# Performance work log

Measured on AMD Instinct MI355X. Metric: run time of the kernel, lower is better.

## Reference

```python
import jax, jax.numpy as jnp
import numpy as np

B, T, E, H = 2, 2048, 1024, 16
D = E // H  # head dim = 64
ROPE_BASE = 10000.0


def setup_inputs() -> dict:
    key = jax.random.key(0)
    k0, k1, k2 = jax.random.split(key, 3)
    s = 0.02  # GPT-style init scale
    return {
        "x": jax.random.normal(k0, (B, T, E), jnp.float32),
        "w_qkv": jax.random.normal(k1, (E, 3 * E), jnp.float32) * s,
        "b_qkv": jnp.zeros((3 * E,), jnp.float32),
        "w_out": jax.random.normal(k2, (E, E), jnp.float32) * s,
        "b_out": jnp.zeros((E,), jnp.float32),
    }


def _rope_tables(t, d, dtype):
    # Llama rotary with scale=1 (YaRN degenerates to vanilla RoPE)
    inv_freq = 1.0 / (ROPE_BASE ** (jnp.arange(0, d, 2, dtype=jnp.float32) / d))
    freqs = jnp.arange(t, dtype=jnp.float32)[:, None] * inv_freq[None, :]  # [T, D/2]
    emb = jnp.concatenate([freqs, freqs], axis=-1)  # [T, D]
    return jnp.cos(emb).astype(dtype), jnp.sin(emb).astype(dtype)


def _rotate_half(x):
    return jnp.concatenate([-x[..., D // 2:], x[..., : D // 2]], axis=-1)


def reference(x, w_qkv, b_qkv, w_out, b_out):
    # 1) fused QKV projection
    qkv = x @ w_qkv + b_qkv                      # [B, T, 3E]
    q, k, v = jnp.split(qkv, 3, axis=-1)

    def heads(t):
        return t.reshape(B, T, H, D).transpose(0, 2, 1, 3)  # [B, H, T, D]

    q, k, v = heads(q), heads(k), heads(v)

    # 2) rotary position embedding on q, k
    cos, sin = _rope_tables(T, D, x.dtype)       # [T, D], broadcasts over B, H
    q = q * cos + _rotate_half(q) * sin
    k = k * cos + _rotate_half(k) * sin

    # 3) causal scaled dot-product attention
    scale = jnp.asarray(1.0 / np.sqrt(D), x.dtype)
    scores = jnp.einsum("bhqd,bhkd->bhqk", q, k) * scale
    causal = jnp.tril(jnp.ones((T, T), dtype=bool))
    scores = jnp.where(causal, scores, jnp.finfo(scores.dtype).min)
    attn = jax.nn.softmax(scores, axis=-1)
    out = jnp.einsum("bhqk,bhkd->bhqd", attn, v)  # [B, H, T, D]

    # 4) merge heads + output projection
    out = out.transpose(0, 2, 1, 3).reshape(B, T, E)
    return out @ w_out + b_out
```

## Files before the change

### kernel.cpp

```cpp
#include <hip/hip_runtime.h>
#include <hip/hip_bf16.h>
#include <stdint.h>

#define B_  2
#define T_  2048
#define E_  1024
#define H_  16
#define D_  64
#define BH_ 32

typedef unsigned short ushort_t;
typedef __attribute__((ext_vector_type(8))) short bfrag;
typedef __attribute__((ext_vector_type(4))) short s16x4;
typedef __attribute__((ext_vector_type(4))) float f32x4;

__device__ __forceinline__ ushort_t f2b(float f) {
    uint32_t u = __builtin_bit_cast(uint32_t, f);
    u += 0x7fffu + ((u >> 16) & 1u);
    return (ushort_t)(u >> 16);
}

#if defined(__has_builtin)
#if __has_builtin(__builtin_amdgcn_exp2f)
#define EXP2(x) __builtin_amdgcn_exp2f(x)
#endif
#endif
#ifndef EXP2
__device__ __forceinline__ float hexp2_(float x) {
    float r;
    asm volatile("v_exp_f32 %0, %1\n\ts_nop 1" : "=v"(r) : "v"(x));
    return r;
}
#define EXP2(x) hexp2_(x)
#endif

__device__ __forceinline__ uint32_t cvtpk_bf16(float lo, float hi) {
    uint32_t r;
    asm("v_cvt_pk_bf16_f32 %0, %1, %2" : "=v"(r) : "v"(lo), "v"(hi));
    return r;
}

typedef const __attribute__((address_space(1))) uint8_t* gas_t;
typedef __attribute__((address_space(3))) uint8_t* las_t;
__device__ __forceinline__ void gload_lds16(const void* g, void* l) {
    __builtin_amdgcn_global_load_lds((gas_t)g, (las_t)l, 16, 0, 0);
}
__device__ __forceinline__ void drain_vmem() {
    asm volatile("s_waitcnt vmcnt(0)" ::: "memory");
    __builtin_amdgcn_sched_barrier(0);
}

__global__ __launch_bounds__(256) void prep_kernel(const float* __restrict__ x, const float* __restrict__ w_qkv,
                                                   const float* __restrict__ w_out, ushort_t* __restrict__ xb,
                                                   ushort_t* __restrict__ wqkvT, ushort_t* __restrict__ woutT,
                                                   float2* __restrict__ cstab) {
    __shared__ float tile[32][36];
    int blk = blockIdx.x, tid = threadIdx.x;
    if (blk < 256) {
        int id = blk * 256 + tid;
        int j = id & 31, t = id >> 5;
        float ang = (float)t * expf(-(float)j * 0.2878231366242558f);
        float s, c;
        sincosf(ang, &s, &c);
        cstab[id] = make_float2(c, s);
    } else if (blk < 2304) {
        int i = ((blk - 256) * 256 + tid) * 8;
        float4 a = *(const float4*)(x + i);
        float4 b = *(const float4*)(x + i + 4);
        ushort_t r[8] = {f2b(a.x), f2b(a.y), f2b(a.z), f2b(a.w), f2b(b.x), f2b(b.y), f2b(b.z), f2b(b.w)};
        *(uint4*)(xb + i) = *(const uint4*)r;
    } else {
        const float* in;
        ushort_t* out;
        int R, C, bx, by;
        if (blk < 5376) { in = w_qkv; out = wqkvT; R = 1024; C = 3072; int t = blk - 2304; bx = t % 96; by = t / 96; }
        else            { in = w_out; out = woutT; R = 1024; C = 1024; int t = blk - 5376; bx = t % 32; by = t / 32; }
        int c0 = bx * 32, r0 = by * 32;
        int ty = tid >> 3, tx = tid & 7;
        float4 v = *(const float4*)&in[(size_t)(r0 + ty) * C + c0 + tx * 4];
        *(float4*)&tile[ty][tx * 4] = v;
        __syncthreads();
        int cc = tid & 31, rq = tid >> 5;
        float t0 = tile[rq * 4 + 0][cc], t1 = tile[rq * 4 + 1][cc];
        float t2 = tile[rq * 4 + 2][cc], t3 = tile[rq * 4 + 3][cc];
        uint2 w;
        w.x = cvtpk_bf16(t0, t1);
        w.y = cvtpk_bf16(t2, t3);
        *(uint2*)&out[(size_t)(c0 + cc) * R + r0 + rq * 4] = w;
    }
}

__global__ __launch_bounds__(256) void gemm_qkv_kernel(const ushort_t* __restrict__ A, const ushort_t* __restrict__ Bt,
                                                       const float* __restrict__ bias, const float2* __restrict__ cstab,
                                                       ushort_t* __restrict__ qw, ushort_t* __restrict__ kw,
                                                       ushort_t* __restrict__ vw) {
    const int K = 1024;
    __shared__ ushort_t As[128 * 64];
    __shared__ ushort_t Bs[128 * 64];
    int tid = threadIdx.x, lane = tid & 63, wid = tid >> 6;
    int lm = lane & 15, lg = lane >> 4;
    int bid = blockIdx.x;
    int xcd = bid & 7, idx = bid >> 3;
    int bm = xcd * 4 + idx / 24;
    int bn = idx % 24;
    int wm = wid >> 1, wn = wid & 1;

    int cbase = bn * 128 + wn * 64;
    bool qk = (cbase < 2048);

    f32x4 acc[4][4] = {};
    const ushort_t* ag = A + (size_t)bm * 128 * K;
    const ushort_t* bg = Bt + (size_t)bn * 128 * K;

    for (int kt = 0; kt < K / 64; ++kt) {
        __syncthreads();
#pragma unroll
        for (int c = 0; c < 4; ++c) {
            int G = c * 256 + tid;
            int rr = G >> 3;
            int gs = (G & 7) ^ (rr & 7);
            gload_lds16(ag + (size_t)rr * K + kt * 64 + gs * 8, As + (c * 256 + wid * 64) * 8);
            gload_lds16(bg + (size_t)rr * K + kt * 64 + gs * 8, Bs + (c * 256 + wid * 64) * 8);
        }
        __syncthreads();
        bfrag a[2][4], b[2][4];
#pragma unroll
        for (int kk = 0; kk < 2; ++kk) {
#pragma unroll
            for (int mi = 0; mi < 4; ++mi) {
                int row = wm * 64 + mi * 16 + lm;
                int slot = (kk * 4 + lg) ^ (lm & 7);
                a[kk][mi] = *(const bfrag*)&As[row * 64 + slot * 8];
            }
#pragma unroll
            for (int ni = 0; ni < 4; ++ni) {
                int row = wn * 64 + ni * 16 + lm;
                int slot = (kk * 4 + lg) ^ (lm & 7);
                b[kk][ni] = *(const bfrag*)&Bs[row * 64 + slot * 8];
            }
        }
        if (qk) {
#pragma unroll
            for (int kk = 0; kk < 2; ++kk)
#pragma unroll
                for (int mi = 0; mi < 4; ++mi)
#pragma unroll
                    for (int ni = 0; ni < 4; ++ni)
                        acc[mi][ni] = __builtin_amdgcn_mfma_f32_16x16x32_bf16(b[kk][ni], a[kk][mi], acc[mi][ni], 0, 0, 0);
        } else {
#pragma unroll
            for (int kk = 0; kk < 2; ++kk)
#pragma unroll
                for (int mi = 0; mi < 4; ++mi)
#pragma unroll
                    for (int ni = 0; ni < 4; ++ni)
                        acc[mi][ni] = __builtin_amdgcn_mfma_f32_16x16x32_bf16(a[kk][mi], b[kk][ni], acc[mi][ni], 0, 0, 0);
        }
    }

    int sel = cbase >> 10;
    int h = (cbase & 1023) >> 6;
    if (qk) {
        ushort_t* dst = sel ? kw : qw;
        float scale = sel ? 1.0f : 0.18033688011112042f;
        float4 bias4[4];
#pragma unroll
        for (int ni = 0; ni < 4; ++ni)
            bias4[ni] = *(const float4*)&bias[cbase + ni * 16 + lg * 4];
#pragma unroll
        for (int mi = 0; mi < 4; ++mi) {
            int r = bm * 128 + wm * 64 + mi * 16 + lm;
            int bb = r >> 11, t = r & (T_ - 1);
            size_t rowbase = ((size_t)(bb * H_ + h) * T_ + t) * D_;
#pragma unroll
            for (int nip = 0; nip < 2; ++nip) {
                const float4* cs2 = (const float4*)(cstab + t * 32 + nip * 16 + lg * 4);
                float4 ca = cs2[0], cb = cs2[1];
                float xl[4], xh[4];
#pragma unroll
                for (int i = 0; i < 4; ++i) {
                    xl[i] = acc[mi][nip][i]     + ((const float*)&bias4[nip])[i];
                    xh[i] = acc[mi][nip + 2][i] + ((const float*)&bias4[nip + 2])[i];
                }
                float rl0 = (xl[0] * ca.x - xh[0] * ca.y) * scale;
                float rl1 = (xl[1] * ca.z - xh[1] * ca.w) * scale;
                float rl2 = (xl[2] * cb.x - xh[2] * cb.y) * scale;
                float rl3 = (xl[3] * cb.z - xh[3] * cb.w) * scale;
                float rh0 = (xh[0] * ca.x + xl[0] * ca.y) * scale;
                float rh1 = (xh[1] * ca.z + xl[1] * ca.w) * scale;
                float rh2 = (xh[2] * cb.x + xl[2] * cb.y) * scale;
                float rh3 = (xh[3] * cb.z + xl[3] * cb.w) * scale;
                uint2 wlo, whi;
                wlo.x = cvtpk_bf16(rl0, rl1); wlo.y = cvtpk_bf16(rl2, rl3);
                whi.x = cvtpk_bf16(rh0, rh1); whi.y = cvtpk_bf16(rh2, rh3);
                *(uint2*)&dst[rowbase + nip * 16 + lg * 4]      = wlo;
                *(uint2*)&dst[rowbase + 32 + nip * 16 + lg * 4] = whi;
            }
        }
    } else {
        float bb4[4];
#pragma unroll
        for (int ni = 0; ni < 4; ++ni) bb4[ni] = bias[cbase + ni * 16 + lm];
#pragma unroll
        for (int ni = 0; ni < 4; ++ni) {
            int d = ni * 16 + lm;
#pragma unroll
            for (int mi = 0; mi < 4; ++mi) {
                int r = bm * 128 + wm * 64 + mi * 16 + lg * 4;
                int bb = r >> 11, tq = r & (T_ - 1);
                uint2 w;
                w.x = cvtpk_bf16(acc[mi][ni][0] + bb4[ni], acc[mi][ni][1] + bb4[ni]);
                w.y = cvtpk_bf16(acc[mi][ni][2] + bb4[ni], acc[mi][ni][3] + bb4[ni]);
                *(uint2*)&vw[((size_t)(bb * H_ + h) * D_ + d) * T_ + tq] = w;
            }
        }
    }
}

__global__ __launch_bounds__(256, 2) void flash_kernel(const ushort_t* __restrict__ q, const ushort_t* __restrict__ k,
                                                       const ushort_t* __restrict__ vt, ushort_t* __restrict__ o) {
    __shared__ ushort_t smemK[128 * 64];
    __shared__ ushort_t smemV[64 * 128];
    int tid = threadIdx.x, lane = tid & 63, wid = tid >> 6;
    int lm = lane & 15, lg = lane >> 4;
    int x = blockIdx.x & 7, r = blockIdx.x >> 3;
    int half = r >> 5, idx = r & 31;
    int bh = x * 4 + (idx & 3);
    int jq = idx >> 2;
    int j = half ? jq : 15 - jq;
    int q0w = j * 128 + wid * 32;
    int b = bh >> 4, h = bh & 15;
    int nt = j + 1;

    const ushort_t* qb = q + (size_t)bh * T_ * D_;
    const ushort_t* kb = k + (size_t)bh * T_ * D_;
    const ushort_t* vb = vt + (size_t)bh * D_ * T_;

    bfrag aq[2][2];
#pragma unroll
    for (int s = 0; s < 2; ++s)
#pragma unroll
        for (int hh = 0; hh < 2; ++hh)
            aq[s][hh] = *(const bfrag*)(qb + (size_t)(q0w + s * 16 + lm) * D_ + hh * 32 + lg * 8);

    f32x4 acc[2][4] = {};
    float lsum[2] = {0.f, 0.f};

    for (int t = 0; t < nt; ++t) {
        int k0 = t * 128;
        __syncthreads();
#pragma unroll
        for (int c = 0; c < 4; ++c) {
            int G = c * 256 + tid;
            int rrk = G >> 3, gk = (G & 7) ^ (rrk & 7);
            gload_lds16(kb + (size_t)(k0 + rrk) * D_ + gk * 8, smemK + (c * 256 + wid * 64) * 8);
            int rrv = G >> 4, gv = (G & 15) ^ (rrv & 7);
            gload_lds16(vb + (size_t)rrv * T_ + k0 + gv * 8, smemV + (c * 256 + wid * 64) * 8);
        }
        drain_vmem();
        __syncthreads();

        for (int h1 = 0; h1 < 2; ++h1) {
            int hk0 = k0 + h1 * 64;
            if (hk0 > q0w + 31) continue;
            bfrag ka[4][2];
#pragma unroll
            for (int sb = 0; sb < 4; ++sb)
#pragma unroll
                for (int hh = 0; hh < 2; ++hh) {
                    int krr = h1 * 64 + sb * 16 + lm;
                    int gr = (hh * 4 + lg) ^ (krr & 7);
                    ka[sb][hh] = *(const bfrag*)&smemK[krr * 64 + gr * 8];
                }
            s16x4 vq[4][4];
#pragma unroll
            for (int qq = 0; qq < 4; ++qq)
#pragma unroll
                for (int db = 0; db < 4; ++db) {
                    int rr = db * 16 + lm;
                    int g = h1 * 8 + qq * 2 + (lg >> 1);
                    int p = g ^ (rr & 7);
                    vq[qq][db] = *(const s16x4*)&smemV[rr * 128 + p * 8 + (lg & 1) * 4];
                }
            f32x4 st[2][4];
#pragma unroll
            for (int s = 0; s < 2; ++s)
#pragma unroll
                for (int sb = 0; sb < 4; ++sb) {
                    f32x4 z = {};
                    z = __builtin_amdgcn_mfma_f32_16x16x32_bf16(ka[sb][0], aq[s][0], z, 0, 0, 0);
                    st[s][sb] = __builtin_amdgcn_mfma_f32_16x16x32_bf16(ka[sb][1], aq[s][1], z, 0, 0, 0);
                }
            if (hk0 + 63 > q0w) {
#pragma unroll
                for (int s = 0; s < 2; ++s)
#pragma unroll
                    for (int sb = 0; sb < 4; ++sb)
#pragma unroll
                        for (int i = 0; i < 4; ++i)
                            if (hk0 + sb * 16 + lg * 4 + i > q0w + s * 16 + lm) st[s][sb][i] = -1e30f;
            }
#pragma unroll
            for (int s = 0; s < 2; ++s) {
                float pv[4][4];
#pragma unroll
                for (int sb = 0; sb < 4; ++sb)
#pragma unroll
                    for (int i = 0; i < 4; ++i)
                        pv[sb][i] = EXP2(st[s][sb][i]);
                lsum[s] += ((pv[0][0] + pv[0][1]) + (pv[0][2] + pv[0][3])) +
                           ((pv[1][0] + pv[1][1]) + (pv[1][2] + pv[1][3])) +
                           ((pv[2][0] + pv[2][1]) + (pv[2][2] + pv[2][3])) +
                           ((pv[3][0] + pv[3][1]) + (pv[3][2] + pv[3][3]));
                uint4 u0, u1;
                u0.x = cvtpk_bf16(pv[0][0], pv[0][1]);
                u0.y = cvtpk_bf16(pv[0][2], pv[0][3]);
                u0.z = cvtpk_bf16(pv[1][0], pv[1][1]);
                u0.w = cvtpk_bf16(pv[1][2], pv[1][3]);
                u1.x = cvtpk_bf16(pv[2][0], pv[2][1]);
                u1.y = cvtpk_bf16(pv[2][2], pv[2][3]);
                u1.z = cvtpk_bf16(pv[3][0], pv[3][1]);
                u1.w = cvtpk_bf16(pv[3][2], pv[3][3]);
                bfrag pf0 = __builtin_bit_cast(bfrag, u0);
                bfrag pf1 = __builtin_bit_cast(bfrag, u1);
#pragma unroll
                for (int db = 0; db < 4; ++db) {
                    bfrag va01 = __builtin_shufflevector(vq[0][db], vq[1][db], 0, 1, 2, 3, 4, 5, 6, 7);
                    bfrag va23 = __builtin_shufflevector(vq[2][db], vq[3][db], 0, 1, 2, 3, 4, 5, 6, 7);
                    acc[s][db] = __builtin_amdgcn_mfma_f32_16x16x32_bf16(va01, pf0, acc[s][db], 0, 0, 0);
                    acc[s][db] = __builtin_amdgcn_mfma_f32_16x16x32_bf16(va23, pf1, acc[s][db], 0, 0, 0);
                }
            }
        }
    }

#pragma unroll
    for (int s = 0; s < 2; ++s) {
        float lM = lsum[s];
        lM += __shfl_xor(lM, 16);
        lM += __shfl_xor(lM, 32);
        float inv = 1.0f / lM;
        int tq = q0w + s * 16 + lm;
        size_t ro = ((size_t)b * T_ + tq) * E_ + h * D_;
#pragma unroll
        for (int db = 0; db < 4; ++db) {
            uint2 w;
            w.x = cvtpk_bf16(acc[s][db][0] * inv, acc[s][db][1] * inv);
            w.y = cvtpk_bf16(acc[s][db][2] * inv, acc[s][db][3] * inv);
            *(uint2*)(o + ro + db * 16 + lg * 4) = w;
        }
    }
}

__global__ __launch_bounds__(256) void gemm_out_kernel(const ushort_t* __restrict__ A, const ushort_t* __restrict__ Bt,
                                                       const float* __restrict__ bias, float* __restrict__ out) {
    const int K = 1024;
    __shared__ ushort_t As[2][128 * 64];
    __shared__ ushort_t Bs[2][64 * 64];
    int tid = threadIdx.x, lane = tid & 63, wid = tid >> 6;
    int lm = lane & 15, lg = lane >> 4;
    int bid = blockIdx.x;
    int xcd = bid & 7, idx = bid >> 3;
    int bm = xcd * 4 + idx / 16;
    int bn = idx % 16;

    f32x4 acc[2][4] = {};
    const ushort_t* ag = A + (size_t)bm * 128 * K;
    const ushort_t* bg = Bt + (size_t)bn * 64 * K;

#define OUT_STAGE(kt_, buf_)                                                              \
    _Pragma("unroll")                                                                     \
    for (int c = 0; c < 4; ++c) {                                                         \
        int G = c * 256 + tid;                                                            \
        int rr = G >> 3;                                                                  \
        int gs = (G & 7) ^ (rr & 7);                                                      \
        gload_lds16(ag + (size_t)rr * K + (kt_) * 64 + gs * 8, &As[buf_][(c * 256 + wid * 64) * 8]); \
    }                                                                                     \
    _Pragma("unroll")                                                                     \
    for (int c = 0; c < 2; ++c) {                                                         \
        int G = c * 256 + tid;                                                            \
        int rr = G >> 3;                                                                  \
        int gs = (G & 7) ^ (rr & 7);                                                      \
        gload_lds16(bg + (size_t)rr * K + (kt_) * 64 + gs * 8, &Bs[buf_][(c * 256 + wid * 64) * 8]); \
    }

    int cur = 0;
    OUT_STAGE(0, 0);
    drain_vmem();
    __syncthreads();

    for (int kt = 0; kt < K / 64; ++kt) {
        if (kt + 1 < K / 64) { OUT_STAGE(kt + 1, cur ^ 1); }
        bfrag a[2][2], b[2][4];
#pragma unroll
        for (int kk = 0; kk < 2; ++kk) {
#pragma unroll
            for (int mi = 0; mi < 2; ++mi) {
                int row = wid * 32 + mi * 16 + lm;
                int slot = (kk * 4 + lg) ^ (lm & 7);
                a[kk][mi] = *(const bfrag*)&As[cur][row * 64 + slot * 8];
            }
#pragma unroll
            for (int ni = 0; ni < 4; ++ni) {
                int row = ni * 16 + lm;
                int slot = (kk * 4 + lg) ^ (lm & 7);
                b[kk][ni] = *(const bfrag*)&Bs[cur][row * 64 + slot * 8];
            }
        }
#pragma unroll
        for (int kk = 0; kk < 2; ++kk)
#pragma unroll
            for (int mi = 0; mi < 2; ++mi)
#pragma unroll
                for (int ni = 0; ni < 4; ++ni)
                    acc[mi][ni] = __builtin_amdgcn_mfma_f32_16x16x32_bf16(a[kk][mi], b[kk][ni], acc[mi][ni], 0, 0, 0);
        drain_vmem();
        __syncthreads();
        cur ^= 1;
    }
#undef OUT_STAGE

#pragma unroll
    for (int ni = 0; ni < 4; ++ni) {
        int c = bn * 64 + ni * 16 + lm;
        float bb = bias[c];
#pragma unroll
        for (int mi = 0; mi < 2; ++mi) {
#pragma unroll
            for (int i = 0; i < 4; ++i) {
                int r = bm * 128 + wid * 32 + mi * 16 + lg * 4 + i;
                out[(size_t)r * 1024 + c] = acc[mi][ni][i] + bb;
            }
        }
    }
}

extern "C" void kernel_launch(void* const* d_in, const int* in_sizes, int n_in,
                              void* d_out, int out_size, void* d_ws, size_t ws_size,
                              hipStream_t stream) {
    const float* x     = (const float*)d_in[0];
    const float* w_qkv = (const float*)d_in[1];
    const float* b_qkv = (const float*)d_in[2];
    const float* w_out = (const float*)d_in[3];
    const float* b_out = (const float*)d_in[4];
    float* out = (float*)d_out;

    ushort_t* ws    = (ushort_t*)d_ws;
    ushort_t* xb    = ws;
    ushort_t* wqkvT = xb + 4194304;
    ushort_t* woutT = wqkvT + 3145728;
    ushort_t* qw    = woutT + 1048576;
    ushort_t* kw    = qw + 4194304;
    ushort_t* vw    = kw + 4194304;
    ushort_t* ao    = vw + 4194304;
    float2*   cstab = (float2*)(ao + 4194304);

    prep_kernel<<<dim3(6400), 256, 0, stream>>>(x, w_qkv, w_out, xb, wqkvT, woutT, cstab);
    gemm_qkv_kernel<<<dim3(768), 256, 0, stream>>>(xb, wqkvT, b_qkv, cstab, qw, kw, vw);
    flash_kernel<<<dim3(512), 256, 0, stream>>>(qw, kw, vw, ao);
    gemm_out_kernel<<<dim3(512), 256, 0, stream>>>(ao, woutT, b_out, out);
}
```

Baseline: 107.3 us.

## Double-buffer QKV GEMM LDS loads and shrink tile to 128x64

```diff
diff --git a/kernel.cpp b/kernel.cpp
--- a/kernel.cpp
+++ b/kernel.cpp
@@ -95,55 +95,65 @@
                                                        ushort_t* __restrict__ qw, ushort_t* __restrict__ kw,
                                                        ushort_t* __restrict__ vw) {
     const int K = 1024;
-    __shared__ ushort_t As[128 * 64];
-    __shared__ ushort_t Bs[128 * 64];
+    __shared__ ushort_t As[2][128 * 64];
+    __shared__ ushort_t Bs[2][64 * 64];
     int tid = threadIdx.x, lane = tid & 63, wid = tid >> 6;
     int lm = lane & 15, lg = lane >> 4;
     int bid = blockIdx.x;
     int xcd = bid & 7, idx = bid >> 3;
-    int bm = xcd * 4 + idx / 24;
-    int bn = idx % 24;
-    int wm = wid >> 1, wn = wid & 1;
-
-    int cbase = bn * 128 + wn * 64;
+    int bm = xcd * 4 + idx / 48;
+    int bn = idx % 48;
+    int cbase = bn * 64;
     bool qk = (cbase < 2048);
 
-    f32x4 acc[4][4] = {};
+    f32x4 acc[2][4] = {};
     const ushort_t* ag = A + (size_t)bm * 128 * K;
-    const ushort_t* bg = Bt + (size_t)bn * 128 * K;
+    const ushort_t* bg = Bt + (size_t)bn * 64 * K;
+
+#define QKV_STAGE(kt_, buf_)                                                              \
+    _Pragma("unroll")                                                                     \
+    for (int c = 0; c < 4; ++c) {                                                         \
+        int G = c * 256 + tid;                                                            \
+        int rr = G >> 3;                                                                  \
+        int gs = (G & 7) ^ (rr & 7);                                                      \
+        gload_lds16(ag + (size_t)rr * K + (kt_) * 64 + gs * 8, &As[buf_][(c * 256 + wid * 64) * 8]); \
+    }                                                                                     \
+    _Pragma("unroll")                                                                     \
+    for (int c = 0; c < 2; ++c) {                                                         \
+        int G = c * 256 + tid;                                                            \
+        int rr = G >> 3;                                                                  \
+        int gs = (G & 7) ^ (rr & 7);                                                      \
+        gload_lds16(bg + (size_t)rr * K + (kt_) * 64 + gs * 8, &Bs[buf_][(c * 256 + wid * 64) * 8]); \
+    }
+
+    int cur = 0;
+    QKV_STAGE(0, 0);
+    drain_vmem();
+    __syncthreads();
 
     for (int kt = 0; kt < K / 64; ++kt) {
-        __syncthreads();
-#pragma unroll
-        for (int c = 0; c < 4; ++c) {
-            int G = c * 256 + tid;
-            int rr = G >> 3;
-            int gs = (G & 7) ^ (rr & 7);
-            gload_lds16(ag + (size_t)rr * K + kt * 64 + gs * 8, As + (c * 256 + wid * 64) * 8);
-            gload_lds16(bg + (size_t)rr * K + kt * 64 + gs * 8, Bs + (c * 256 + wid * 64) * 8);
-        }
-        __syncthreads();
-        bfrag a[2][4], b[2][4];
+        if (kt + 1 < K / 64) { QKV_STAGE(kt + 1, cur ^ 1); }
+        bfrag a[2][2], b[2][4];
 #pragma unroll
         for (int kk = 0; kk < 2; ++kk) {
 #pragma unroll
-            for (int mi = 0; mi < 4; ++mi) {
-                int row = wm * 64 + mi * 16 + lm;
+            for (int mi = 0; mi < 2; ++mi) {
+                int row = wid * 32 + mi * 16 + lm;
                 int slot = (kk * 4 + lg) ^ (lm & 7);
-                a[kk][mi] = *(const bfrag*)&As[row * 64 + slot * 8];
+                a[kk][mi] = *(const bfrag*)&As[cur][row * 64 + slot * 8];
             }
 #pragma unroll
             for (int ni = 0; ni < 4; ++ni) {
-                int row = wn * 64 + ni * 16 + lm;
+                int row = ni * 16 + lm;
                 int slot = (kk * 4 + lg) ^ (lm & 7);
-                b[kk][ni] = *(const bfrag*)&Bs[row * 64 + slot * 8];
+                b[kk][ni] = *(const bfrag*)&Bs[cur][row * 64 + slot * 8];
             }
         }
         if (qk) {
 #pragma unroll
             for (int kk = 0; kk < 2; ++kk)
 #pragma unroll
-                for (int mi = 0; mi < 4; ++mi)
+                for (int mi = 0; mi < 2; ++mi)
 #pragma unroll
                     for (int ni = 0; ni < 4; ++ni)
                         acc[mi][ni] = __builtin_amdgcn_mfma_f32_16x16x32_bf16(b[kk][ni], a[kk][mi], acc[mi][ni], 0, 0, 0);
@@ -151,12 +161,16 @@
 #pragma unroll
             for (int kk = 0; kk < 2; ++kk)
 #pragma unroll
-                for (int mi = 0; mi < 4; ++mi)
+                for (int mi = 0; mi < 2; ++mi)
 #pragma unroll
                     for (int ni = 0; ni < 4; ++ni)
                         acc[mi][ni] = __builtin_amdgcn_mfma_f32_16x16x32_bf16(a[kk][mi], b[kk][ni], acc[mi][ni], 0, 0, 0);
         }
-    }
+        drain_vmem();
+        __syncthreads();
+        cur ^= 1;
+    }
+#undef QKV_STAGE
 
     int sel = cbase >> 10;
     int h = (cbase & 1023) >> 6;
@@ -168,8 +182,8 @@
         for (int ni = 0; ni < 4; ++ni)
             bias4[ni] = *(const float4*)&bias[cbase + ni * 16 + lg * 4];
 #pragma unroll
-        for (int mi = 0; mi < 4; ++mi) {
-            int r = bm * 128 + wm * 64 + mi * 16 + lm;
+        for (int mi = 0; mi < 2; ++mi) {
+            int r = bm * 128 + wid * 32 + mi * 16 + lm;
             int bb = r >> 11, t = r & (T_ - 1);
             size_t rowbase = ((size_t)(bb * H_ + h) * T_ + t) * D_;
 #pragma unroll
@@ -205,8 +219,8 @@
         for (int ni = 0; ni < 4; ++ni) {
             int d = ni * 16 + lm;
 #pragma unroll
-            for (int mi = 0; mi < 4; ++mi) {
-                int r = bm * 128 + wm * 64 + mi * 16 + lg * 4;
+            for (int mi = 0; mi < 2; ++mi) {
+                int r = bm * 128 + wid * 32 + mi * 16 + lg * 4;
                 int bb = r >> 11, tq = r & (T_ - 1);
                 uint2 w;
                 w.x = cvtpk_bf16(acc[mi][ni][0] + bb4[ni], acc[mi][ni][1] + bb4[ni]);
@@ -456,7 +470,7 @@
     float2*   cstab = (float2*)(ao + 4194304);
 
     prep_kernel<<<dim3(6400), 256, 0, stream>>>(x, w_qkv, w_out, xb, wqkvT, woutT, cstab);
-    gemm_qkv_kernel<<<dim3(768), 256, 0, stream>>>(xb, wqkvT, b_qkv, cstab, qw, kw, vw);
+    gemm_qkv_kernel<<<dim3(1536), 256, 0, stream>>>(xb, wqkvT, b_qkv, cstab, qw, kw, vw);
     flash_kernel<<<dim3(512), 256, 0, stream>>>(qw, kw, vw, ao);
     gemm_out_kernel<<<dim3(512), 256, 0, stream>>>(ao, woutT, b_out, out);
 }
```

After: 119.2 us. 11.0% more time.
